# Performance work log

Hardware: AMD Instinct MI355X
Metric: run time of the kernel (lower is better)

Reference implementation:

```python
import jax, jax.numpy as jnp
import numpy as np

B, L, V, E, H2, M, OOV = 128, 400, 50000, 512, 1024, 1024, 50


def setup_inputs() -> dict:
    key = jax.random.key(0)
    ks = jax.random.split(key, 14)
    s = 0.02
    return {
        "y": jax.random.randint(ks[0], (B,), 0, V),
        "h": jax.random.normal(ks[1], (1, B, H2), jnp.float32),
        "memory_bank": jax.random.normal(ks[2], (B, L, M), jnp.float32),
        "src_mask": jnp.ones((B, L), jnp.float32),
        "max_num_oovs": OOV,
        "src_oov": jax.random.randint(ks[3], (B, L), 0, V + OOV),
        # learned parameters (PyTorch Linear y = x @ W + b with W stored [in, out])
        "emb": jax.random.normal(ks[4], (V, E), jnp.float32) * s,
        "W_ih": jax.random.normal(ks[5], (E, 3 * H2), jnp.float32) * s,   # GRU input weights (r|z|n)
        "W_hh": jax.random.normal(ks[6], (H2, 3 * H2), jnp.float32) * s,  # GRU hidden weights (r|z|n)
        "b_ih": jnp.zeros((3 * H2,), jnp.float32),
        "b_hh": jnp.zeros((3 * H2,), jnp.float32),
        "W_mem": jax.random.normal(ks[7], (M, H2), jnp.float32) * s,      # attention memory_project (no bias)
        "W_dec": jax.random.normal(ks[8], (H2, H2), jnp.float32) * s,     # attention decode_project
        "b_dec": jnp.zeros((H2,), jnp.float32),
        "v": jax.random.normal(ks[9], (H2,), jnp.float32) * s,            # attention score vector (no bias)
        "W_pgen": jax.random.normal(ks[10], (M + H2 + E, 1), jnp.float32) * s,
        "b_pgen": jnp.zeros((1,), jnp.float32),
        "W_v1": jax.random.normal(ks[11], (M + H2, H2), jnp.float32) * s,
        "b_v1": jnp.zeros((H2,), jnp.float32),
        "W_v2": jax.random.normal(ks[12], (H2, V), jnp.float32) * s,
        "b_v2": jnp.zeros((V,), jnp.float32),
    }


def reference(y, h, memory_bank, src_mask, max_num_oovs, src_oov,
              emb, W_ih, W_hh, b_ih, b_hh, W_mem, W_dec, b_dec, v,
              W_pgen, b_pgen, W_v1, b_v1, W_v2, b_v2):
    # --- embedding lookup (single decode step) ---
    y_emb = emb[y]                                    # [B, E]
    h0 = h[-1]                                        # [B, H2]

    # --- one-step GRU (PyTorch gate order r, z, n); dropout is identity (eval) ---
    gi = y_emb @ W_ih + b_ih                          # [B, 3*H2]
    gh = h0 @ W_hh + b_hh
    i_r, i_z, i_n = jnp.split(gi, 3, axis=-1)
    h_r, h_z, h_n = jnp.split(gh, 3, axis=-1)
    r = jax.nn.sigmoid(i_r + h_r)
    z = jax.nn.sigmoid(i_z + h_z)
    n = jnp.tanh(i_n + r * h_n)
    h_next = (1.0 - z) * n + z * h0                   # [B, H2]

    # --- concat (Bahdanau) attention with masked softmax ---
    enc_feat = jnp.einsum('blm,mh->blh', memory_bank, W_mem)   # [B, L, H2]
    dec_feat = h_next @ W_dec + b_dec                           # [B, H2]
    scores = jnp.tanh(enc_feat + dec_feat[:, None, :]) @ v     # [B, L]
    attn = jax.nn.softmax(scores, axis=1) * src_mask
    attn_dist = attn / attn.sum(axis=1, keepdims=True)         # renormalized masked softmax
    context = jnp.einsum('bl,blm->bm', attn_dist, memory_bank) # [B, M]

    # --- vocab distribution ---
    vd_in = jnp.concatenate([context, h_next], axis=1)          # [B, M+H2]
    logits = (vd_in @ W_v1 + b_v1) @ W_v2 + b_v2                # [B, V]
    vocab_dist = jax.nn.softmax(logits, axis=1)

    # --- generation gate ---
    pg_in = jnp.concatenate([context, h_next, y_emb], axis=1)   # [B, M+H2+E]
    p_gen = jax.nn.sigmoid(pg_in @ W_pgen + b_pgen)             # [B, 1]

    # --- copy mechanism: scatter attention mass into extended vocab ---
    vocab_dist_ = p_gen * vocab_dist
    attn_dist_ = (1.0 - p_gen) * attn_dist
    bsz = vocab_dist_.shape[0]
    if max_num_oovs > 0:
        vocab_dist_ = jnp.concatenate(
            [vocab_dist_, jnp.zeros((bsz, max_num_oovs), vocab_dist_.dtype)], axis=1)
    rows = jnp.arange(bsz)[:, None]
    final_dist = vocab_dist_.at[rows, src_oov].add(attn_dist_)  # [B, V+OOV]

    return final_dist, h_next[None], context, attn_dist, p_gen
```

## Files before the change

### kernel.cpp

```cpp
#include <hip/hip_runtime.h>

#define B_   128
#define L_   400
#define V_   50000
#define E_   512
#define H2_  1024
#define M_   1024
#define OOV_ 50
#define VE_  50050
#define BL_  51200

typedef __attribute__((ext_vector_type(8))) short short8;
typedef __attribute__((ext_vector_type(4))) float f32x4;

__device__ __forceinline__ unsigned short f2bf(float f){
  unsigned int u = __builtin_bit_cast(unsigned int, f);
  u = (u + 0x7FFFu + ((u >> 16) & 1u)) >> 16;
  return (unsigned short)u;
}
__device__ __forceinline__ float bf2f(unsigned short s){
  unsigned int u = ((unsigned int)s) << 16;
  return __builtin_bit_cast(float, u);
}

__device__ __forceinline__ void gl_lds16(const void* g, void* l){
  __builtin_amdgcn_global_load_lds(
      (const __attribute__((address_space(1))) unsigned int*)g,
      (__attribute__((address_space(3))) unsigned int*)l, 16, 0, 0);
}

__device__ __forceinline__ float wredsum(float v){
  #pragma unroll
  for (int o = 32; o > 0; o >>= 1) v += __shfl_xor(v, o);
  return v;
}
__device__ __forceinline__ float wredmax(float v){
  #pragma unroll
  for (int o = 32; o > 0; o >>= 1) v = fmaxf(v, __shfl_xor(v, o));
  return v;
}

__device__ __forceinline__ void mb_convert_unit(const float* __restrict__ mb,
                                                unsigned char* __restrict__ mbT, int u){
  int gr  = u >> 7;
  int m16 = u & 127;
  const float* src = mb + (size_t)gr * 1024 + m16 * 8;
  float4 f0 = *(const float4*)src;
  float4 f1 = *(const float4*)(src + 4);
  uint4 w;
  w.x = (unsigned)f2bf(f0.x) | ((unsigned)f2bf(f0.y) << 16);
  w.y = (unsigned)f2bf(f0.z) | ((unsigned)f2bf(f0.w) << 16);
  w.z = (unsigned)f2bf(f1.x) | ((unsigned)f2bf(f1.y) << 16);
  w.w = (unsigned)f2bf(f1.z) | ((unsigned)f2bf(f1.w) << 16);
  int panel = gr >> 7, r = gr & 127;
  int ks = m16 >> 3, c16 = m16 & 7;
  size_t dst = (size_t)panel * 262144 + (size_t)ks * 16384
             + (size_t)((r * 128 + c16 * 16) ^ ((r & 7) << 4));
  *(uint4*)(mbT + dst) = w;
}

__global__ void pre_kernel(const float* __restrict__ mb, unsigned char* __restrict__ mbT,
                           const float* __restrict__ Wm, unsigned char* __restrict__ WTt,
                           const int* __restrict__ y, const float* __restrict__ emb,
                           float* __restrict__ yemb, float* __restrict__ zeroA,
                           float* __restrict__ ctx)
{
  __shared__ float tile[32][33];
  int bid = blockIdx.x, t = threadIdx.x;
  if (bid < 6400){
    mb_convert_unit(mb, mbT, bid * 256 + t);
  } else if (bid < 7424){
    int b2 = bid - 6400;
    int n0 = (b2 & 31) * 32, k0 = (b2 >> 5) * 32;
    int tx = t & 31, ty = t >> 5;
    #pragma unroll
    for (int i = 0; i < 32; i += 8) tile[ty + i][tx] = Wm[(size_t)(k0 + ty + i) * H2_ + n0 + tx];
    __syncthreads();
    if (t < 128){
      int nn = t & 31, k16 = t >> 5;
      int col = n0 + nn, kb = k0 + k16 * 8;
      uint4 w;
      w.x = (unsigned)f2bf(tile[k16*8+0][nn]) | ((unsigned)f2bf(tile[k16*8+1][nn]) << 16);
      w.y = (unsigned)f2bf(tile[k16*8+2][nn]) | ((unsigned)f2bf(tile[k16*8+3][nn]) << 16);
      w.z = (unsigned)f2bf(tile[k16*8+4][nn]) | ((unsigned)f2bf(tile[k16*8+5][nn]) << 16);
      w.w = (unsigned)f2bf(tile[k16*8+6][nn]) | ((unsigned)f2bf(tile[k16*8+7][nn]) << 16);
      int cpn = col >> 7, r = col & 127;
      int ks = kb >> 6, c16 = (kb & 63) >> 3;
      size_t dst = (size_t)cpn * 262144 + (size_t)ks * 16384
                 + (size_t)((r * 128 + c16 * 16) ^ ((r & 7) << 4));
      *(uint4*)(WTt + dst) = w;
    }
  } else if (bid < 7488){
    int idx = (bid - 7424) * 256 + t;
    int b  = idx >> 7;
    int c4 = (idx & 127) << 2;
    float4 v = *(const float4*)(emb + (size_t)y[b] * E_ + c4);
    *(float4*)(yemb + (size_t)b * E_ + c4) = v;
  } else if (bid < 8434){
    int u = (bid - 7488) * 256 + t;
    float4 z = {0.f, 0.f, 0.f, 0.f};
    *(float4*)(zeroA + (size_t)u * 4) = z;
  } else {
    int u = (bid - 8434) * 256 + t;
    float4 z = {0.f, 0.f, 0.f, 0.f};
    *(float4*)(ctx + (size_t)u * 4) = z;
  }
}

__device__ __forceinline__ void gemm128_body(int bx, int by,
                               const float* __restrict__ A, int lda,
                               const float* __restrict__ W, int ldw,
                               const float* __restrict__ bias,
                               float* __restrict__ C, int ldc,
                               int N, int kChunk, int addBias)
{
  int tid = threadIdx.x;
  int wv = tid >> 6, lane = tid & 63, lr = lane & 15, lhi = lane >> 4;
  int colBase = bx * 128 + wv * 32;
  int colL[2];
  colL[0] = min(colBase + lr, N - 1);
  colL[1] = min(colBase + 16 + lr, N - 1);
  int k0 = by * kChunk;

  f32x4 zero = {0.f, 0.f, 0.f, 0.f};
  f32x4 acc[8][2];
  #pragma unroll
  for (int r = 0; r < 8; r++){ acc[r][0] = zero; acc[r][1] = zero; }

  int nks = kChunk >> 5;
  for (int ks = 0; ks < nks; ++ks){
    int k = k0 + ks * 32 + lhi * 8;
    short8 bf[2];
    #pragma unroll
    for (int cf = 0; cf < 2; cf++){
      #pragma unroll
      for (int j = 0; j < 8; j++)
        bf[cf][j] = (short)f2bf(W[(size_t)(k + j) * ldw + colL[cf]]);
    }
    #pragma unroll
    for (int rf = 0; rf < 8; rf++){
      const float* ap = A + (size_t)(rf * 16 + lr) * lda + k;
      float4 a0 = *(const float4*)ap;
      float4 a1 = *(const float4*)(ap + 4);
      short8 af;
      af[0]=(short)f2bf(a0.x); af[1]=(short)f2bf(a0.y); af[2]=(short)f2bf(a0.z); af[3]=(short)f2bf(a0.w);
      af[4]=(short)f2bf(a1.x); af[5]=(short)f2bf(a1.y); af[6]=(short)f2bf(a1.z); af[7]=(short)f2bf(a1.w);
      acc[rf][0] = __builtin_amdgcn_mfma_f32_16x16x32_bf16(af, bf[0], acc[rf][0], 0, 0, 0);
      acc[rf][1] = __builtin_amdgcn_mfma_f32_16x16x32_bf16(af, bf[1], acc[rf][1], 0, 0, 0);
    }
  }

  bool addB = addBias && (by == 0);
  #pragma unroll
  for (int cf = 0; cf < 2; cf++){
    int col = colBase + cf * 16 + lr;
    bool ok = col < N;
    float bv = addB ? bias[colL[cf]] : 0.f;
    #pragma unroll
    for (int rf = 0; rf < 8; rf++)
      #pragma unroll
      for (int i = 0; i < 4; i++){
        int row = rf * 16 + lhi * 4 + i;
        if (ok) atomicAdd(&C[(size_t)row * ldc + col], acc[rf][cf][i] + bv);
      }
  }
}

__launch_bounds__(256)
__global__ void gigh_kernel(const float* __restrict__ yemb, const float* __restrict__ hin,
                            const float* __restrict__ W_ih, const float* __restrict__ W_hh,
                            float* __restrict__ gi, float* __restrict__ gh,
                            const float* __restrict__ mb, unsigned char* __restrict__ mbT){
  int bid = blockIdx.x;
  if (bid < 48)
    gemm128_body(bid % 24, bid / 24, yemb, E_,  W_ih, 3 * H2_, nullptr, gi, 3 * H2_, 3 * H2_, 256, 0);
  else if (bid < 144){
    int b2 = bid - 48;
    gemm128_body(b2 % 24, b2 / 24, hin, H2_, W_hh, 3 * H2_, nullptr, gh, 3 * H2_, 3 * H2_, 256, 0);
  } else {
    mb_convert_unit(mb, mbT, (6400 + bid - 144) * 256 + threadIdx.x);
  }
}

__global__ void gru_gates_kernel(const float* __restrict__ gi, const float* __restrict__ gh,
                                 const float* __restrict__ bih, const float* __restrict__ bhh,
                                 const float* __restrict__ h0, float* __restrict__ hn,
                                 const float* __restrict__ mb, unsigned char* __restrict__ mbT){
  int bid = blockIdx.x;
  if (bid >= 512){
    mb_convert_unit(mb, mbT, (12800 + bid - 512) * 256 + threadIdx.x);
    return;
  }
  int idx = bid * 256 + threadIdx.x;
  int b = idx >> 10, j = idx & 1023;
  const float* gib = gi + (size_t)b * 3072;
  const float* ghb = gh + (size_t)b * 3072;
  float ir = gib[j]        + bih[j],        hr = ghb[j]        + bhh[j];
  float iz = gib[j + 1024] + bih[j + 1024], hz = ghb[j + 1024] + bhh[j + 1024];
  float in_= gib[j + 2048] + bih[j + 2048], hnv= ghb[j + 2048] + bhh[j + 2048];
  float r = 1.f / (1.f + __expf(-(ir + hr)));
  float z = 1.f / (1.f + __expf(-(iz + hz)));
  float n = tanhf(in_ + r * hnv);
  hn[idx] = (1.f - z) * n + z * h0[idx];
}

__launch_bounds__(256)
__global__ void dec_kernel(const float* __restrict__ hnext, const float* __restrict__ W_dec,
                           const float* __restrict__ b_dec, float* __restrict__ dec,
                           const float* __restrict__ mb, unsigned char* __restrict__ mbT){
  int bid = blockIdx.x;
  if (bid < 32)
    gemm128_body(bid & 7, bid >> 3, hnext, H2_, W_dec, H2_, b_dec, dec, H2_, H2_, 256, 1);
  else
    mb_convert_unit(mb, mbT, (19200 + bid - 32) * 256 + threadIdx.x);
}

__launch_bounds__(256)
__global__ void scores_kernel(const unsigned char* __restrict__ mbT,
                              const unsigned char* __restrict__ WTt,
                              const float* __restrict__ dec, const float* __restrict__ vvec,
                              float* __restrict__ scr)
{
  __shared__ __align__(16) unsigned char LDSm[65536];
  const int tid = threadIdx.x, lane = tid & 63;
  const int wv = tid >> 6, lr = lane & 15, lhi = lane >> 4;
  const int wru = wv >> 1, wcu = wv & 1;

  int p = blockIdx.x;
  int lid = (p & 7) * 400 + (p >> 3);
  int rp = lid >> 3, cp = lid & 7;
  int r0 = rp << 7;

  int wvu = __builtin_amdgcn_readfirstlane(wv);
  const unsigned char* segA = mbT + (size_t)rp * 262144 + wvu * 4096 + lane * 16;
  const unsigned char* segB = WTt + (size_t)cp * 262144 + wvu * 4096 + lane * 16;
  const int ldsA = wvu * 4096;
  const int ldsB = 16384 + wvu * 4096;

  int aoff[4], boff[4];
  #pragma unroll
  for (int rf = 0; rf < 4; rf++){
    int row = wru * 64 + rf * 16 + lr;
    aoff[rf] = (row * 128 + lhi * 16) ^ ((row & 7) << 4);
  }
  #pragma unroll
  for (int cf = 0; cf < 4; cf++){
    int col = wcu * 64 + cf * 16 + lr;
    boff[cf] = ((col * 128 + lhi * 16) ^ ((col & 7) << 4)) + 16384;
  }

  f32x4 zero = {0.f, 0.f, 0.f, 0.f};
  f32x4 acc[4][4];
  #pragma unroll
  for (int rf = 0; rf < 4; rf++)
    #pragma unroll
    for (int cf = 0; cf < 4; cf++) acc[rf][cf] = zero;

  #pragma unroll
  for (int j = 0; j < 4; j++){
    gl_lds16(segA + j * 1024, &LDSm[ldsA + j * 1024]);
    gl_lds16(segB + j * 1024, &LDSm[ldsB + j * 1024]);
  }

  #pragma unroll 1
  for (int t = 0; t < 16; ++t){
    const int cur = (t & 1) << 15;
    if (t < 15){
      const size_t soff = (size_t)(t + 1) * 16384;
      const int nb = ((t + 1) & 1) << 15;
      #pragma unroll
      for (int j = 0; j < 4; j++){
        gl_lds16(segA + soff + j * 1024, &LDSm[nb + ldsA + j * 1024]);
        gl_lds16(segB + soff + j * 1024, &LDSm[nb + ldsB + j * 1024]);
      }
      asm volatile("s_waitcnt vmcnt(8)" ::: "memory");
    } else {
      asm volatile("s_waitcnt vmcnt(0)" ::: "memory");
    }
    __builtin_amdgcn_s_barrier();
    __builtin_amdgcn_sched_barrier(0);

    #pragma unroll
    for (int k2 = 0; k2 < 2; k2++){
      short8 af[4], bfr[4];
      #pragma unroll
      for (int rf = 0; rf < 4; rf++) af[rf]  = *(const short8*)&LDSm[cur + (aoff[rf] ^ (k2 << 6))];
      #pragma unroll
      for (int cf = 0; cf < 4; cf++) bfr[cf] = *(const short8*)&LDSm[cur + (boff[cf] ^ (k2 << 6))];
      #pragma unroll
      for (int rf = 0; rf < 4; rf++)
        #pragma unroll
        for (int cf = 0; cf < 4; cf++)
          acc[rf][cf] = __builtin_amdgcn_mfma_f32_16x16x32_bf16(af[rf], bfr[cf], acc[rf][cf], 0, 0, 0);
    }

    __builtin_amdgcn_sched_barrier(0);
    __builtin_amdgcn_s_barrier();
    __builtin_amdgcn_sched_barrier(0);
  }

  int colb = (cp << 7) + wcu * 64 + lr;
  float vv0 = vvec[colb], vv1 = vvec[colb + 16], vv2 = vvec[colb + 32], vv3 = vvec[colb + 48];
  #pragma unroll
  for (int rf = 0; rf < 4; rf++){
    #pragma unroll
    for (int i = 0; i < 4; i++){
      int grow = r0 + wru * 64 + rf * 16 + lhi * 4 + i;
      int bb = grow / 400;
      const float* dp = dec + (size_t)bb * 1024 + colb;
      float x0 = acc[rf][0][i] + dp[0];
      float x1 = acc[rf][1][i] + dp[16];
      float x2 = acc[rf][2][i] + dp[32];
      float x3 = acc[rf][3][i] + dp[48];
      float part = (1.f - 2.f / (__expf(2.f * x0) + 1.f)) * vv0
                 + (1.f - 2.f / (__expf(2.f * x1) + 1.f)) * vv1
                 + (1.f - 2.f / (__expf(2.f * x2) + 1.f)) * vv2
                 + (1.f - 2.f / (__expf(2.f * x3) + 1.f)) * vv3;
      part += __shfl_xor(part, 1);
      part += __shfl_xor(part, 2);
      part += __shfl_xor(part, 4);
      part += __shfl_xor(part, 8);
      if (lr == 0) atomicAdd(&scr[grow], part);
    }
  }
}

__launch_bounds__(256)
__global__ void context_kernel(const float* __restrict__ scr, const float* __restrict__ mask,
                               const unsigned char* __restrict__ mbT,
                               float* __restrict__ ctx, float* __restrict__ attn){
  int b = blockIdx.y, lc = blockIdx.x, t = threadIdx.x;
  int wv = t >> 6, lane = t & 63;
  __shared__ float red[4];
  __shared__ float a[400];
  float s0 = scr[b * 400 + t];
  float s1 = (t < 144) ? scr[b * 400 + t + 256] : -1e30f;
  float m = wredmax(fmaxf(s0, s1));
  if (lane == 0) red[wv] = m;
  __syncthreads();
  float M = fmaxf(fmaxf(red[0], red[1]), fmaxf(red[2], red[3]));
  __syncthreads();
  float e0 = __expf(s0 - M) * mask[b * 400 + t];
  float e1 = (t < 144) ? __expf(s1 - M) * mask[b * 400 + t + 256] : 0.f;
  float s = wredsum(e0 + e1);
  if (lane == 0) red[wv] = s;
  __syncthreads();
  float inv = 1.f / (red[0] + red[1] + red[2] + red[3]);
  a[t] = e0 * inv;
  if (t < 144) a[t + 256] = e1 * inv;
  __syncthreads();
  if (t < 100) attn[b * 400 + lc * 100 + t] = a[lc * 100 + t];

  int u = t & 127;
  int half = t >> 7;
  int ks = u >> 3, c16 = u & 7;
  float sa[8];
  #pragma unroll
  for (int j = 0; j < 8; j++) sa[j] = 0.f;
  for (int l = half; l < 100; l += 2){
    int gr = b * 400 + lc * 100 + l;
    int panel = gr >> 7, r = gr & 127;
    const unsigned char* pp = mbT + (size_t)panel * 262144 + (size_t)ks * 16384
                              + (size_t)((r * 128 + c16 * 16) ^ ((r & 7) << 4));
    short8 v = *(const short8*)pp;
    float al = a[lc * 100 + l];
    #pragma unroll
    for (int j = 0; j < 8; j++) sa[j] += al * bf2f((unsigned short)v[j]);
  }
  float* cp = ctx + (size_t)b * M_ + u * 8;
  #pragma unroll
  for (int j = 0; j < 8; j++) atomicAdd(cp + j, sa[j]);
}

__launch_bounds__(256)
__global__ void v1_pgen_kernel(const float* __restrict__ ctx, const float* __restrict__ hn,
                               const float* __restrict__ yemb,
                               const float* __restrict__ Wv1, const float* __restrict__ bv1,
                               float* __restrict__ vp,
                               const float* __restrict__ Wp, const float* __restrict__ bp,
                               float* __restrict__ pg)
{
  int bid = blockIdx.x;
  if (bid < 64){
    int bx = bid & 7, by = bid >> 3;
    int tid = threadIdx.x;
    int wv = tid >> 6, lane = tid & 63, lr = lane & 15, lhi = lane >> 4;
    int colBase = bx * 128 + wv * 32;
    const float* Asrc = (by < 4) ? ctx : hn;
    int k0 = ((by < 4) ? by : (by - 4)) * 256;
    int wk0 = by * 256;

    f32x4 zero = {0.f, 0.f, 0.f, 0.f};
    f32x4 acc[8][2];
    #pragma unroll
    for (int r = 0; r < 8; r++){ acc[r][0] = zero; acc[r][1] = zero; }

    for (int ks = 0; ks < 8; ++ks){
      int k  = k0 + ks * 32 + lhi * 8;
      int wk = wk0 + ks * 32 + lhi * 8;
      short8 bf[2];
      #pragma unroll
      for (int cf = 0; cf < 2; cf++){
        #pragma unroll
        for (int j = 0; j < 8; j++)
          bf[cf][j] = (short)f2bf(Wv1[(size_t)(wk + j) * H2_ + colBase + cf * 16 + lr]);
      }
      #pragma unroll
      for (int rf = 0; rf < 8; rf++){
        const float* ap = Asrc + (size_t)(rf * 16 + lr) * 1024 + k;
        float4 a0 = *(const float4*)ap;
        float4 a1 = *(const float4*)(ap + 4);
        short8 af;
        af[0]=(short)f2bf(a0.x); af[1]=(short)f2bf(a0.y); af[2]=(short)f2bf(a0.z); af[3]=(short)f2bf(a0.w);
        af[4]=(short)f2bf(a1.x); af[5]=(short)f2bf(a1.y); af[6]=(short)f2bf(a1.z); af[7]=(short)f2bf(a1.w);
        acc[rf][0] = __builtin_amdgcn_mfma_f32_16x16x32_bf16(af, bf[0], acc[rf][0], 0, 0, 0);
        acc[rf][1] = __builtin_amdgcn_mfma_f32_16x16x32_bf16(af, bf[1], acc[rf][1], 0, 0, 0);
      }
    }

    float* Cw = vp + (size_t)by * 131072;
    bool addB = (by == 0);
    #pragma unroll
    for (int cf = 0; cf < 2; cf++){
      int col = colBase + cf * 16 + lr;
      float bv = addB ? bv1[col] : 0.f;
      #pragma unroll
      for (int rf = 0; rf < 8; rf++)
        #pragma unroll
        for (int i = 0; i < 4; i++){
          int row = rf * 16 + lhi * 4 + i;
          Cw[(size_t)row * H2_ + col] = acc[rf][cf][i] + bv;
        }
    }
  } else {
    int b = bid - 64, t = threadIdx.x, wv = t >> 6, lane = t & 63;
    __shared__ float red[4];
    float s = 0.f;
    for (int i = t; i < 1024; i += 256) s += ctx[(size_t)b * 1024 + i] * Wp[i];
    for (int i = t; i < 1024; i += 256) s += hn[(size_t)b * 1024 + i] * Wp[1024 + i];
    for (int i = t; i < 512;  i += 256) s += yemb[(size_t)b * 512 + i] * Wp[2048 + i];
    s = wredsum(s);
    if (lane == 0) red[wv] = s;
    __syncthreads();
    if (t == 0){
      float S = red[0] + red[1] + red[2] + red[3] + bp[0];
      pg[b] = 1.f / (1.f + __expf(-S));
    }
  }
}

__global__ void hid2bf_kernel(const float* __restrict__ vp, unsigned short* __restrict__ hb){
  int id = blockIdx.x * 256 + threadIdx.x;
  float4 s = *(const float4*)(vp + (size_t)id * 4);
  #pragma unroll
  for (int ky = 1; ky < 8; ky++){
    float4 v = *(const float4*)(vp + (size_t)ky * 131072 + (size_t)id * 4);
    s.x += v.x; s.y += v.y; s.z += v.z; s.w += v.w;
  }
  ushort2 p0 = {f2bf(s.x), f2bf(s.y)};
  ushort2 p1 = {f2bf(s.z), f2bf(s.w)};
  *(ushort2*)(hb + (size_t)id * 4)     = p0;
  *(ushort2*)(hb + (size_t)id * 4 + 2) = p1;
}

__launch_bounds__(256)
__global__ void gemm_bfA_kernel(const unsigned short* __restrict__ A,
                                const float* __restrict__ W,
                                const float* __restrict__ bias,
                                float* __restrict__ C, int N)
{
  int tid = threadIdx.x;
  int wv = tid >> 6, lane = tid & 63, lr = lane & 15, lhi = lane >> 4;
  int colBase = blockIdx.x * 128 + wv * 32;
  int colL[2];
  colL[0] = min(colBase + lr, N - 1);
  colL[1] = min(colBase + 16 + lr, N - 1);

  f32x4 zero = {0.f, 0.f, 0.f, 0.f};
  f32x4 acc[8][2];
  #pragma unroll
  for (int r = 0; r < 8; r++){ acc[r][0] = zero; acc[r][1] = zero; }

  for (int ks = 0; ks < 32; ++ks){
    int k = ks * 32 + lhi * 8;
    short8 bf[2];
    #pragma unroll
    for (int cf = 0; cf < 2; cf++){
      #pragma unroll
      for (int j = 0; j < 8; j++)
        bf[cf][j] = (short)f2bf(W[(size_t)(k + j) * N + colL[cf]]);
    }
    #pragma unroll
    for (int rf = 0; rf < 8; rf++){
      short8 af = *(const short8*)(A + (size_t)(rf * 16 + lr) * 1024 + k);
      acc[rf][0] = __builtin_amdgcn_mfma_f32_16x16x32_bf16(af, bf[0], acc[rf][0], 0, 0, 0);
      acc[rf][1] = __builtin_amdgcn_mfma_f32_16x16x32_bf16(af, bf[1], acc[rf][1], 0, 0, 0);
    }
  }

  #pragma unroll
  for (int cf = 0; cf < 2; cf++){
    int col = colBase + cf * 16 + lr;
    bool ok = col < N;
    float bv = bias[colL[cf]];
    #pragma unroll
    for (int rf = 0; rf < 8; rf++)
      #pragma unroll
      for (int i = 0; i < 4; i++){
        int row = rf * 16 + lhi * 4 + i;
        if (ok) C[(size_t)row * V_ + col] = acc[rf][cf][i] + bv;
      }
  }
}

__global__ void vocab_softmax_kernel(const float* __restrict__ lg0, const float* __restrict__ pg,
                                     const float* __restrict__ attn, const int* __restrict__ soov,
                                     float* __restrict__ fin){
  int b = blockIdx.x, t = threadIdx.x, wv = t >> 6, lane = t & 63;
  __shared__ float redm[16], reds[16];
  const float* l0 = lg0 + (size_t)b * V_;
  float m = -1e30f, s = 0.f;
  for (int i = t; i < V_; i += 1024){
    float l = l0[i];
    float mn = fmaxf(m, l);
    s = s * __expf(m - mn) + __expf(l - mn);
    m = mn;
  }
  #pragma unroll
  for (int o = 32; o > 0; o >>= 1){
    float mo = __shfl_xor(m, o), so = __shfl_xor(s, o);
    float mn = fmaxf(m, mo);
    s = s * __expf(m - mn) + so * __expf(mo - mn);
    m = mn;
  }
  if (lane == 0){ redm[wv] = m; reds[wv] = s; }
  __syncthreads();
  float M = -1e30f;
  #pragma unroll
  for (int w = 0; w < 16; w++) M = fmaxf(M, redm[w]);
  float S = 0.f;
  #pragma unroll
  for (int w = 0; w < 16; w++) S += reds[w] * __expf(redm[w] - M);
  float pgb = pg[b];
  float scale = pgb / S;
  float* fb = fin + (size_t)b * VE_;
  for (int i = t; i < V_; i += 1024) fb[i] = __expf(l0[i] - M) * scale;
  for (int i = V_ + t; i < VE_; i += 1024) fb[i] = 0.f;
  __syncthreads();
  float om = 1.f - pgb;
  if (t < 400) atomicAdd(&fb[soov[b * 400 + t]], om * attn[b * 400 + t]);
}

extern "C" void kernel_launch(void* const* d_in, const int* in_sizes, int n_in,
                              void* d_out, int out_size, void* d_ws, size_t ws_size,
                              hipStream_t stream)
{
  const int*   y     = (const int*)  d_in[0];
  const float* hin   = (const float*)d_in[1];
  const float* mb    = (const float*)d_in[2];
  const float* mask  = (const float*)d_in[3];
  const int*   soov  = (const int*)  d_in[5];
  const float* emb   = (const float*)d_in[6];
  const float* W_ih  = (const float*)d_in[7];
  const float* W_hh  = (const float*)d_in[8];
  const float* b_ih  = (const float*)d_in[9];
  const float* b_hh  = (const float*)d_in[10];
  const float* W_mem = (const float*)d_in[11];
  const float* W_dec = (const float*)d_in[12];
  const float* b_dec = (const float*)d_in[13];
  const float* vvec  = (const float*)d_in[14];
  const float* W_pg  = (const float*)d_in[15];
  const float* b_pg  = (const float*)d_in[16];
  const float* W_v1  = (const float*)d_in[17];
  const float* b_v1  = (const float*)d_in[18];
  const float* W_v2  = (const float*)d_in[19];
  const float* b_v2  = (const float*)d_in[20];

  float* out   = (float*)d_out;
  float* fin   = out;
  float* hnext = out + (size_t)B_ * VE_;
  float* ctx   = hnext + (size_t)B_ * H2_;
  float* attn  = ctx + (size_t)B_ * M_;
  float* pg    = attn + (size_t)B_ * L_;

  float* ws   = (float*)d_ws;
  float* yemb = ws;
  float* gi   = ws + 65536;
  float* gh   = gi + 393216;
  float* dec  = gh + 393216;
  float* scr  = dec + 131072;
  float* lg0  = scr + 51200;
  float* vp   = lg0;
  unsigned short* hidbf = (unsigned short*)(lg0 + 6400000);
  unsigned char*  WTt   = (unsigned char*)(hidbf + 131072);
  unsigned char*  mbT   = WTt + 2097152;

  pre_kernel<<<8562, 256, 0, stream>>>(mb, mbT, W_mem, WTt, y, emb, yemb, gi, ctx);
  gigh_kernel<<<6544, 256, 0, stream>>>(yemb, hin, W_ih, W_hh, gi, gh, mb, mbT);
  gru_gates_kernel<<<6912, 256, 0, stream>>>(gi, gh, b_ih, b_hh, hin, hnext, mb, mbT);
  dec_kernel<<<6432, 256, 0, stream>>>(hnext, W_dec, b_dec, dec, mb, mbT);

  scores_kernel<<<3200, 256, 0, stream>>>(mbT, WTt, dec, vvec, scr);
  context_kernel<<<dim3(4, 128), 256, 0, stream>>>(scr, mask, mbT, ctx, attn);

  v1_pgen_kernel<<<192, 256, 0, stream>>>(ctx, hnext, yemb, W_v1, b_v1, vp, W_pg, b_pg, pg);
  hid2bf_kernel<<<128, 256, 0, stream>>>(vp, hidbf);
  gemm_bfA_kernel<<<391, 256, 0, stream>>>(hidbf, W_v2, b_v2, lg0, V_);

  vocab_softmax_kernel<<<128, 1024, 0, stream>>>(lg0, pg, attn, soov, fin);
}
```

Baseline: 504.1 us.

## Replace LDS DMA pipeline with register staging and per-column-block score partials

The scores GEMM drops its double-buffered global_load_lds pipeline. It now loads tiles into registers, then writes them to a single LDS buffer between barriers, which halves LDS use so more blocks can be resident. Atomic adds into the score array are replaced by 16 partial-score slots per row that the context kernel sums, so the zero-init of the score buffer shrinks. The W_v2 bf16 conversion switches from round-to-nearest to truncation, which is cheaper but slightly less accurate.

Measured after the change: 901.0 us. 78.7% more time.

```diff
diff --git a/kernel.cpp b/kernel.cpp
--- a/kernel.cpp
+++ b/kernel.cpp
@@ -22,11 +22,8 @@
   unsigned int u = ((unsigned int)s) << 16;
   return __builtin_bit_cast(float, u);
 }
-
-__device__ __forceinline__ void gl_lds16(const void* g, void* l){
-  __builtin_amdgcn_global_load_lds(
-      (const __attribute__((address_space(1))) unsigned int*)g,
-      (__attribute__((address_space(3))) unsigned int*)l, 16, 0, 0);
+__device__ __forceinline__ short f2bf_t(float f){
+  return (short)(__builtin_bit_cast(unsigned int, f) >> 16);
 }
 
 __device__ __forceinline__ float wredsum(float v){
@@ -96,12 +93,12 @@
     int c4 = (idx & 127) << 2;
     float4 v = *(const float4*)(emb + (size_t)y[b] * E_ + c4);
     *(float4*)(yemb + (size_t)b * E_ + c4) = v;
-  } else if (bid < 8434){
+  } else if (bid < 8384){
     int u = (bid - 7488) * 256 + t;
     float4 z = {0.f, 0.f, 0.f, 0.f};
     *(float4*)(zeroA + (size_t)u * 4) = z;
   } else {
-    int u = (bid - 8434) * 256 + t;
+    int u = (bid - 8384) * 256 + t;
     float4 z = {0.f, 0.f, 0.f, 0.f};
     *(float4*)(ctx + (size_t)u * 4) = z;
   }
@@ -219,9 +216,9 @@
 __global__ void scores_kernel(const unsigned char* __restrict__ mbT,
                               const unsigned char* __restrict__ WTt,
                               const float* __restrict__ dec, const float* __restrict__ vvec,
-                              float* __restrict__ scr)
+                              float* __restrict__ scrp)
 {
-  __shared__ __align__(16) unsigned char LDSm[65536];
+  __shared__ __align__(16) unsigned char LDSm[32768];
   const int tid = threadIdx.x, lane = tid & 63;
   const int wv = tid >> 6, lr = lane & 15, lhi = lane >> 4;
   const int wru = wv >> 1, wcu = wv & 1;
@@ -234,8 +231,8 @@
   int wvu = __builtin_amdgcn_readfirstlane(wv);
   const unsigned char* segA = mbT + (size_t)rp * 262144 + wvu * 4096 + lane * 16;
   const unsigned char* segB = WTt + (size_t)cp * 262144 + wvu * 4096 + lane * 16;
-  const int ldsA = wvu * 4096;
-  const int ldsB = 16384 + wvu * 4096;
+  const int ldsA = wvu * 4096 + lane * 16;
+  const int ldsB = 16384 + wvu * 4096 + lane * 16;
 
   int aoff[4], boff[4];
   #pragma unroll
@@ -256,47 +253,51 @@
     #pragma unroll
     for (int cf = 0; cf < 4; cf++) acc[rf][cf] = zero;
 
+  uint4 ra[4], rb[4];
   #pragma unroll
   for (int j = 0; j < 4; j++){
-    gl_lds16(segA + j * 1024, &LDSm[ldsA + j * 1024]);
-    gl_lds16(segB + j * 1024, &LDSm[ldsB + j * 1024]);
-  }
+    ra[j] = *(const uint4*)(segA + j * 1024);
+    rb[j] = *(const uint4*)(segB + j * 1024);
+  }
+  #pragma unroll
+  for (int j = 0; j < 4; j++){
+    *(uint4*)&LDSm[ldsA + j * 1024] = ra[j];
+    *(uint4*)&LDSm[ldsB + j * 1024] = rb[j];
+  }
+  __syncthreads();
 
   #pragma unroll 1
   for (int t = 0; t < 16; ++t){
-    const int cur = (t & 1) << 15;
     if (t < 15){
       const size_t soff = (size_t)(t + 1) * 16384;
-      const int nb = ((t + 1) & 1) << 15;
       #pragma unroll
       for (int j = 0; j < 4; j++){
-        gl_lds16(segA + soff + j * 1024, &LDSm[nb + ldsA + j * 1024]);
-        gl_lds16(segB + soff + j * 1024, &LDSm[nb + ldsB + j * 1024]);
+        ra[j] = *(const uint4*)(segA + soff + j * 1024);
+        rb[j] = *(const uint4*)(segB + soff + j * 1024);
       }
-      asm volatile("s_waitcnt vmcnt(8)" ::: "memory");
-    } else {
-      asm volatile("s_waitcnt vmcnt(0)" ::: "memory");
-    }
-    __builtin_amdgcn_s_barrier();
-    __builtin_amdgcn_sched_barrier(0);
-
+    }
     #pragma unroll
     for (int k2 = 0; k2 < 2; k2++){
       short8 af[4], bfr[4];
       #pragma unroll
-      for (int rf = 0; rf < 4; rf++) af[rf]  = *(const short8*)&LDSm[cur + (aoff[rf] ^ (k2 << 6))];
-      #pragma unroll
-      for (int cf = 0; cf < 4; cf++) bfr[cf] = *(const short8*)&LDSm[cur + (boff[cf] ^ (k2 << 6))];
+      for (int rf = 0; rf < 4; rf++) af[rf]  = *(const short8*)&LDSm[aoff[rf] ^ (k2 << 6)];
+      #pragma unroll
+      for (int cf = 0; cf < 4; cf++) bfr[cf] = *(const short8*)&LDSm[boff[cf] ^ (k2 << 6)];
       #pragma unroll
       for (int rf = 0; rf < 4; rf++)
         #pragma unroll
         for (int cf = 0; cf < 4; cf++)
           acc[rf][cf] = __builtin_amdgcn_mfma_f32_16x16x32_bf16(af[rf], bfr[cf], acc[rf][cf], 0, 0, 0);
     }
-
-    __builtin_amdgcn_sched_barrier(0);
-    __builtin_amdgcn_s_barrier();
-    __builtin_amdgcn_sched_barrier(0);
+    __syncthreads();
+    if (t < 15){
+      #pragma unroll
+      for (int j = 0; j < 4; j++){
+        *(uint4*)&LDSm[ldsA + j * 1024] = ra[j];
+        *(uint4*)&LDSm[ldsB + j * 1024] = rb[j];
+      }
+      __syncthreads();
+    }
   }
 
   int colb = (cp << 7) + wcu * 64 + lr;
@@ -320,21 +321,32 @@
       part += __shfl_xor(part, 2);
       part += __shfl_xor(part, 4);
       part += __shfl_xor(part, 8);
-      if (lr == 0) atomicAdd(&scr[grow], part);
+      if (lr == 0) scrp[(size_t)grow * 16 + cp * 2 + wcu] = part;
     }
   }
 }
 
 __launch_bounds__(256)
-__global__ void context_kernel(const float* __restrict__ scr, const float* __restrict__ mask,
+__global__ void context_kernel(const float* __restrict__ scrp, const float* __restrict__ mask,
                                const unsigned char* __restrict__ mbT,
                                float* __restrict__ ctx, float* __restrict__ attn){
   int b = blockIdx.y, lc = blockIdx.x, t = threadIdx.x;
   int wv = t >> 6, lane = t & 63;
   __shared__ float red[4];
   __shared__ float a[400];
-  float s0 = scr[b * 400 + t];
-  float s1 = (t < 144) ? scr[b * 400 + t + 256] : -1e30f;
+  int row0 = b * 400 + t;
+  float s0 = 0.f, s1;
+  {
+    const float4* p0 = (const float4*)(scrp + (size_t)row0 * 16);
+    #pragma unroll
+    for (int q = 0; q < 4; q++){ float4 v = p0[q]; s0 += v.x + v.y + v.z + v.w; }
+    if (t < 144){
+      s1 = 0.f;
+      const float4* p1 = (const float4*)(scrp + (size_t)(row0 + 256) * 16);
+      #pragma unroll
+      for (int q = 0; q < 4; q++){ float4 v = p1[q]; s1 += v.x + v.y + v.z + v.w; }
+    } else s1 = -1e30f;
+  }
   float m = wredmax(fmaxf(s0, s1));
   if (lane == 0) red[wv] = m;
   __syncthreads();
@@ -488,7 +500,7 @@
     for (int cf = 0; cf < 2; cf++){
       #pragma unroll
       for (int j = 0; j < 8; j++)
-        bf[cf][j] = (short)f2bf(W[(size_t)(k + j) * N + colL[cf]]);
+        bf[cf][j] = f2bf_t(W[(size_t)(k + j) * N + colL[cf]]);
     }
     #pragma unroll
     for (int rf = 0; rf < 8; rf++){
@@ -588,20 +600,20 @@
   float* gi   = ws + 65536;
   float* gh   = gi + 393216;
   float* dec  = gh + 393216;
-  float* scr  = dec + 131072;
-  float* lg0  = scr + 51200;
+  float* scrp = dec + 131072;
+  float* lg0  = scrp + 819200;
   float* vp   = lg0;
   unsigned short* hidbf = (unsigned short*)(lg0 + 6400000);
   unsigned char*  WTt   = (unsigned char*)(hidbf + 131072);
   unsigned char*  mbT   = WTt + 2097152;
 
-  pre_kernel<<<8562, 256, 0, stream>>>(mb, mbT, W_mem, WTt, y, emb, yemb, gi, ctx);
+  pre_kernel<<<8512, 256, 0, stream>>>(mb, mbT, W_mem, WTt, y, emb, yemb, gi, ctx);
   gigh_kernel<<<6544, 256, 0, stream>>>(yemb, hin, W_ih, W_hh, gi, gh, mb, mbT);
   gru_gates_kernel<<<6912, 256, 0, stream>>>(gi, gh, b_ih, b_hh, hin, hnext, mb, mbT);
   dec_kernel<<<6432, 256, 0, stream>>>(hnext, W_dec, b_dec, dec, mb, mbT);
 
-  scores_kernel<<<3200, 256, 0, stream>>>(mbT, WTt, dec, vvec, scr);
-  context_kernel<<<dim3(4, 128), 256, 0, stream>>>(scr, mask, mbT, ctx, attn);
+  scores_kernel<<<3200, 256, 0, stream>>>(mbT, WTt, dec, vvec, scrp);
+  context_kernel<<<dim3(4, 128), 256, 0, stream>>>(scrp, mask, mbT, ctx, attn);
 
   v1_pgen_kernel<<<192, 256, 0, stream>>>(ctx, hnext, yemb, W_v1, b_v1, vp, W_pg, b_pg, pg);
   hid2bf_kernel<<<128, 256, 0, stream>>>(vp, hidbf);
```
